# Kernel tuning notes

Measured on AMD Instinct MI355X. Metric: run time of the kernel, lower is better.

## Reference

```python
import jax, jax.numpy as jnp
import numpy as np

B, T, C, H = 8, 2048, 1024, 128

def setup_inputs() -> dict:
    key = jax.random.key(0)
    kx, kq, kk, kv = jax.random.split(key, 4)
    x = jax.random.normal(kx, (B, T, C), dtype=jnp.float32)
    Wq = jax.random.normal(kq, (C, H), dtype=jnp.float32) * 0.02
    Wk = jax.random.normal(kk, (C, H), dtype=jnp.float32) * 0.02
    Wv = jax.random.normal(kv, (C, H), dtype=jnp.float32) * 0.02
    return {"x": x, "Wq": Wq, "Wk": Wk, "Wv": Wv}

def reference(x, Wq, Wk, Wv):
    # q,k,v: [B,T,H] via bias-free dense projections
    q = jnp.einsum('btc,ch->bth', x, Wq)
    k = jnp.einsum('btc,ch->bth', x, Wk)
    v = jnp.einsum('btc,ch->bth', x, Wv)
    scale = k.shape[-1] ** (-0.5)
    # scores: [B,T,T]
    wei = jnp.einsum('bth,bsh->bts', q, k) * scale
    Tlen = x.shape[1]
    causal = jnp.tril(jnp.ones((Tlen, Tlen), dtype=bool))  # True = keep
    wei = jnp.where(causal[None, :, :], wei, -jnp.inf)
    wei = jax.nn.softmax(wei, axis=-1)
    return jnp.einsum('bts,bsh->bth', wei, v)
```

## Files before the change

kernel.cpp:

```cpp
#include <hip/hip_runtime.h>

#define B_ 8
#define T_ 2048
#define C_ 1024
#define H_ 128
#define BT_ (B_*T_)

typedef unsigned short u16;
typedef unsigned int u32;
typedef __attribute__((ext_vector_type(4))) float f32x4;
typedef __attribute__((ext_vector_type(8))) __bf16 bf16x8;

__device__ __forceinline__ u16 f2bf(float f) {
  u32 u = __float_as_uint(f);
  u += 0x7fffu + ((u >> 16) & 1u);
  return (u16)(u >> 16);
}

__device__ __forceinline__ void dma16(const u16* g, u16* l) {
  __builtin_amdgcn_global_load_lds(
      (const __attribute__((address_space(1))) u32*)g,
      (__attribute__((address_space(3))) u32*)l, 16, 0, 0);
}

__device__ __forceinline__ bf16x8 load_frag(const u16* base, int stride, int row0, int k0, int lane) {
  const u16* p = base + (size_t)(row0 + (lane & 15)) * stride + k0 + ((lane >> 4) << 3);
  return *reinterpret_cast<const bf16x8*>(p);
}

__global__ __launch_bounds__(256) void prep_kernel(const float* __restrict__ x,
                                                   const float* __restrict__ Wq,
                                                   const float* __restrict__ Wk,
                                                   const float* __restrict__ Wv,
                                                   u16* __restrict__ xb, u16* __restrict__ wt) {
  __shared__ float tile[32][33];
  int blk = blockIdx.x, t = threadIdx.x;
  if (blk < 2048) {
    size_t base = (size_t)blk * 8192 + t * 8;
#pragma unroll
    for (int j = 0; j < 4; j++) {
      size_t i = base + (size_t)j * 2048;
      float4 a = *reinterpret_cast<const float4*>(x + i);
      float4 b = *reinterpret_cast<const float4*>(x + i + 4);
      union { u16 h[8]; uint4 v; } r;
      r.h[0] = f2bf(a.x); r.h[1] = f2bf(a.y); r.h[2] = f2bf(a.z); r.h[3] = f2bf(a.w);
      r.h[4] = f2bf(b.x); r.h[5] = f2bf(b.y); r.h[6] = f2bf(b.z); r.h[7] = f2bf(b.w);
      *reinterpret_cast<uint4*>(xb + i) = r.v;
    }
  } else {
    int tid = blk - 2048;
    int mat = tid >> 7;
    int rem = tid & 127;
    int c0 = (rem & 31) * 32;
    int h0 = (rem >> 5) * 32;
    const float* W = (mat == 0) ? Wq : (mat == 1) ? Wk : Wv;
    int rr = t >> 5, cc = t & 31;
#pragma unroll
    for (int p = 0; p < 4; p++) {
      int i = p * 8 + rr;
      tile[i][cc] = W[(size_t)(c0 + i) * H_ + h0 + cc];
    }
    __syncthreads();
#pragma unroll
    for (int p = 0; p < 4; p++) {
      int j = p * 8 + rr;
      wt[(size_t)mat * (C_ * H_) + (size_t)(h0 + j) * C_ + c0 + cc] = f2bf(tile[cc][j]);
    }
  }
}

__global__ __launch_bounds__(256) void qkv_gemm(const u16* __restrict__ xb, const u16* __restrict__ wt,
                                                u16* __restrict__ q, u16* __restrict__ k2,
                                                u16* __restrict__ vt) {
  __shared__ __align__(16) u16 As[2][4096];
  __shared__ __align__(16) u16 Bs[2][4096];
  int t = threadIdx.x;
  int lane = t & 63, w = t >> 6;
  int wm = w >> 1, wn = w & 1;
  int quad = lane >> 4, col = lane & 15;
  int m0 = blockIdx.x * 128;
  int mat = blockIdx.y;
  const u16* wtm = wt + mat * (C_ * H_);

  int rj[2], oj[2];
#pragma unroll
  for (int j = 0; j < 2; j++) {
    int c = (j * 4 + w) * 64 + lane;
    int r = c >> 2;
    int qg = (c & 3) ^ ((r >> 1) & 3);
    rj[j] = r; oj[j] = qg * 8;
  }

#pragma unroll
  for (int j = 0; j < 2; j++) {
    dma16(xb + (size_t)(m0 + rj[j]) * C_ + oj[j], &As[0][(j * 4 + w) * 512]);
    dma16(wtm + (size_t)rj[j] * C_ + oj[j], &Bs[0][(j * 4 + w) * 512]);
  }

  int aoff[4], boff[4];
#pragma unroll
  for (int mt = 0; mt < 4; mt++) {
    int row = wm * 64 + mt * 16 + col;
    aoff[mt] = (4 * row + (quad ^ ((row >> 1) & 3))) * 8;
    int rowb = wn * 64 + mt * 16 + col;
    boff[mt] = (4 * rowb + (quad ^ ((rowb >> 1) & 3))) * 8;
  }

  f32x4 acc[4][4] = {};
  for (int kk = 0; kk < 32; kk++) {
    int cur = kk & 1;
    __syncthreads();
    if (kk + 1 < 32) {
      int nxt = cur ^ 1;
      int kn = (kk + 1) * 32;
#pragma unroll
      for (int j = 0; j < 2; j++) {
        dma16(xb + (size_t)(m0 + rj[j]) * C_ + kn + oj[j], &As[nxt][(j * 4 + w) * 512]);
        dma16(wtm + (size_t)rj[j] * C_ + kn + oj[j], &Bs[nxt][(j * 4 + w) * 512]);
      }
    }
    bf16x8 af[4], bfr[4];
#pragma unroll
    for (int mt = 0; mt < 4; mt++) af[mt] = *reinterpret_cast<const bf16x8*>(&As[cur][aoff[mt]]);
#pragma unroll
    for (int nt = 0; nt < 4; nt++) bfr[nt] = *reinterpret_cast<const bf16x8*>(&Bs[cur][boff[nt]]);
#pragma unroll
    for (int mt = 0; mt < 4; mt++)
#pragma unroll
      for (int nt = 0; nt < 4; nt++)
        acc[mt][nt] = __builtin_amdgcn_mfma_f32_16x16x32_bf16(af[mt], bfr[nt], acc[mt][nt], 0, 0, 0);
  }

#pragma unroll
  for (int mt = 0; mt < 4; mt++) {
#pragma unroll
    for (int nt = 0; nt < 4; nt++) {
#pragma unroll
      for (int r = 0; r < 4; r++) {
        int row = m0 + wm * 64 + mt * 16 + quad * 4 + r;
        int n = wn * 64 + nt * 16 + col;
        u16 val = f2bf(acc[mt][nt][r]);
        if (mat == 0) {
          q[(size_t)row * H_ + n] = val;
        } else if (mat == 1) {
          k2[(size_t)row * H_ + n] = val;
        } else {
          int bb = row >> 11;
          int tt = row & 2047;
          vt[((size_t)bb * H_ + n) * T_ + tt] = val;
        }
      }
    }
  }
}

__global__ __launch_bounds__(256) void attn_part(const u16* __restrict__ q, const u16* __restrict__ k,
                                                 const u16* __restrict__ vt,
                                                 float* __restrict__ Op, float* __restrict__ lsum) {
  __shared__ __align__(16) u16 Ks[2][8192];
  __shared__ __align__(16) u16 Vs[2][8192];
  __shared__ __align__(16) u16 P[4][16 * 72];
  int t = threadIdx.x;
  int lane = t & 63, w = t >> 6;
  int quad = lane >> 4, col = lane & 15;
  int bx = blockIdx.x;
  int qt = 31 - (bx >> 4);
  int s = (bx >> 3) & 1;
  int b = bx & 7;
  const float scale = 0.08838834764831845f;

  int nkt = qt + 1;
  int n0 = (nkt + 1) >> 1;
  int it0 = s ? n0 : 0;
  int it1 = s ? nkt : n0;

  int krj[4], koj[4], vrj[4], voj[4];
#pragma unroll
  for (int j = 0; j < 4; j++) {
    int c = (j * 4 + w) * 64 + lane;
    int rk = c >> 4; krj[j] = rk; koj[j] = ((c & 15) ^ (rk & 7)) * 8;
    int rv = c >> 3; vrj[j] = rv; voj[j] = ((c & 7) ^ (rv & 7)) * 8;
  }

  int qrow0 = b * T_ + qt * 64 + w * 16;
  bf16x8 qf[4];
#pragma unroll
  for (int ks = 0; ks < 4; ks++) qf[ks] = load_frag(q, H_, qrow0, ks * 32, lane);

  int koff[4][4], voff[8][2];
#pragma unroll
  for (int g = 0; g < 4; g++) {
    int row = g * 16 + col;
#pragma unroll
    for (int ks = 0; ks < 4; ks++)
      koff[g][ks] = (16 * row + ((ks * 4 + quad) ^ (row & 7))) * 8;
  }
#pragma unroll
  for (int ht = 0; ht < 8; ht++) {
    int row = ht * 16 + col;
#pragma unroll
    for (int kk = 0; kk < 2; kk++)
      voff[ht][kk] = (8 * row + ((kk * 4 + quad) ^ (row & 7))) * 8;
  }

  f32x4 o[8] = {};
  float l[4] = {0.f, 0.f, 0.f, 0.f};
  int myqrow = qt * 64 + w * 16 + quad * 4;
  u16* Pb = &P[w][0];

  if (it0 < it1) {
    {
      const u16* kb = k + (size_t)(b * T_ + it0 * 64) * H_;
      const u16* vb = vt + (size_t)b * H_ * T_ + it0 * 64;
#pragma unroll
      for (int j = 0; j < 4; j++) {
        dma16(kb + (size_t)krj[j] * H_ + koj[j], &Ks[0][(j * 4 + w) * 512]);
        dma16(vb + (size_t)vrj[j] * T_ + voj[j], &Vs[0][(j * 4 + w) * 512]);
      }
    }

    for (int kt = it0; kt < it1; kt++) {
      int cur = (kt - it0) & 1;
      __syncthreads();
      if (kt + 1 < it1) {
        int nxt = cur ^ 1;
        const u16* kb = k + (size_t)(b * T_ + (kt + 1) * 64) * H_;
        const u16* vb = vt + (size_t)b * H_ * T_ + (kt + 1) * 64;
#pragma unroll
        for (int j = 0; j < 4; j++) {
          dma16(kb + (size_t)krj[j] * H_ + koj[j], &Ks[nxt][(j * 4 + w) * 512]);
          dma16(vb + (size_t)vrj[j] * T_ + voj[j], &Vs[nxt][(j * 4 + w) * 512]);
        }
      }

      f32x4 sg[4] = {};
#pragma unroll
      for (int g = 0; g < 4; g++) {
#pragma unroll
        for (int ks = 0; ks < 4; ks++) {
          bf16x8 kf = *reinterpret_cast<const bf16x8*>(&Ks[cur][koff[g][ks]]);
          sg[g] = __builtin_amdgcn_mfma_f32_16x16x32_bf16(qf[ks], kf, sg[g], 0, 0, 0);
        }
      }

      bool diag = (kt == nkt - 1);
      float pv[4][4];
#pragma unroll
      for (int g = 0; g < 4; g++) {
        int kcol = kt * 64 + g * 16 + col;
#pragma unroll
        for (int r = 0; r < 4; r++) {
          float a = fminf(sg[g][r] * scale, 30.f);
          if (diag) a = (kcol > myqrow + r) ? -1e30f : a;
          float p = __expf(a);
          pv[g][r] = p;
          l[r] += p;
        }
      }

#pragma unroll
      for (int g = 0; g < 4; g++)
#pragma unroll
        for (int r = 0; r < 4; r++)
          Pb[(quad * 4 + r) * 72 + g * 16 + col] = f2bf(pv[g][r]);
      asm volatile("" ::: "memory");
      __builtin_amdgcn_s_waitcnt(0xc07f);
      asm volatile("" ::: "memory");
      bf16x8 pf0 = *reinterpret_cast<const bf16x8*>(&Pb[col * 72 + quad * 8]);
      bf16x8 pf1 = *reinterpret_cast<const bf16x8*>(&Pb[col * 72 + 32 + quad * 8]);

#pragma unroll
      for (int ht = 0; ht < 8; ht++) {
        bf16x8 vf0 = *reinterpret_cast<const bf16x8*>(&Vs[cur][voff[ht][0]]);
        bf16x8 vf1 = *reinterpret_cast<const bf16x8*>(&Vs[cur][voff[ht][1]]);
        o[ht] = __builtin_amdgcn_mfma_f32_16x16x32_bf16(pf0, vf0, o[ht], 0, 0, 0);
        o[ht] = __builtin_amdgcn_mfma_f32_16x16x32_bf16(pf1, vf1, o[ht], 0, 0, 0);
      }
    }
  }

#pragma unroll
  for (int r = 0; r < 4; r++) {
    float v = l[r];
    v += __shfl_xor(v, 1);
    v += __shfl_xor(v, 2);
    v += __shfl_xor(v, 4);
    v += __shfl_xor(v, 8);
    l[r] = v;
  }

  int tile = (s * 8 + b) * 32 + qt;
  float* Orow = Op + (size_t)tile * (64 * 128);
  float* lrow = lsum + (size_t)tile * 64;
  int rowin0 = w * 16 + quad * 4;
  if (col == 0) {
#pragma unroll
    for (int r = 0; r < 4; r++) lrow[rowin0 + r] = l[r];
  }
#pragma unroll
  for (int ht = 0; ht < 8; ht++) {
#pragma unroll
    for (int r = 0; r < 4; r++)
      Orow[(size_t)(rowin0 + r) * 128 + ht * 16 + col] = o[ht][r];
  }
}

__global__ __launch_bounds__(256) void attn_comb(const float* __restrict__ Op, const float* __restrict__ lsum,
                                                 float* __restrict__ out) {
  int bx = blockIdx.x;
  int b = bx >> 5, qt = bx & 31;
  int t = threadIdx.x;
  int h = t & 127, half = t >> 7;
  int tile0 = b * 32 + qt;
  int tile1 = tile0 + 256;
#pragma unroll 4
  for (int rr = 0; rr < 32; rr++) {
    int row = half * 32 + rr;
    float l0 = lsum[tile0 * 64 + row];
    float l1 = lsum[tile1 * 64 + row];
    float rl = 1.f / (l0 + l1);
    float v = (Op[(size_t)tile0 * 8192 + row * 128 + h] +
               Op[(size_t)tile1 * 8192 + row * 128 + h]) * rl;
    out[((size_t)(b * T_ + qt * 64 + row)) * H_ + h] = v;
  }
}

extern "C" void kernel_launch(void* const* d_in, const int* in_sizes, int n_in,
                              void* d_out, int out_size, void* d_ws, size_t ws_size,
                              hipStream_t stream) {
  (void)in_sizes; (void)n_in; (void)out_size; (void)ws_size;
  const float* x  = (const float*)d_in[0];
  const float* Wq = (const float*)d_in[1];
  const float* Wk = (const float*)d_in[2];
  const float* Wv = (const float*)d_in[3];
  u16* ws = (u16*)d_ws;
  u16* xb = ws;
  u16* q  = ws + (size_t)BT_ * C_;
  u16* k  = q + (size_t)BT_ * H_;
  u16* vt = k + (size_t)BT_ * H_;
  u16* wt = vt + (size_t)BT_ * H_;
  float* Op = (float*)xb;
  float* lsum = Op + (size_t)512 * 64 * 128;
  float* out = (float*)d_out;

  prep_kernel<<<dim3(2432), 256, 0, stream>>>(x, Wq, Wk, Wv, xb, wt);
  qkv_gemm<<<dim3(128, 3), 256, 0, stream>>>(xb, wt, q, k, vt);
  attn_part<<<dim3(512), 256, 0, stream>>>(q, k, vt, Op, lsum);
  attn_comb<<<dim3(256), 256, 0, stream>>>(Op, lsum, out);
}
```

Before: 175.0 us.

## Fuse split-KV combine into attention via atomic tickets, shrink QKV GEMM tiles

Removes the separate combine kernel. Each attention block bumps a per-tile atomic counter after writing its partial result, and the second finisher merges both halves and writes the final output. The counters are zeroed inside the prep kernel. The QKV GEMM M-tile is halved to 64 rows, doubling the block count for better CU occupancy. Block order is also remapped so the heaviest causal tiles of the two splits interleave, which should balance the load. In exchange it adds threadfence and atomic traffic and relies on correct cross-block memory ordering.

Result: slower. 260.4 us (+48.8%).

```diff
diff --git a/kernel.cpp b/kernel.cpp
--- a/kernel.cpp
+++ b/kernel.cpp
@@ -32,7 +32,8 @@
                                                    const float* __restrict__ Wq,
                                                    const float* __restrict__ Wk,
                                                    const float* __restrict__ Wv,
-                                                   u16* __restrict__ xb, u16* __restrict__ wt) {
+                                                   u16* __restrict__ xb, u16* __restrict__ wt,
+                                                   int* __restrict__ tick) {
   __shared__ float tile[32][33];
   int blk = blockIdx.x, t = threadIdx.x;
   if (blk < 2048) {
@@ -49,6 +50,7 @@
     }
   } else {
     int tid = blk - 2048;
+    if (tid == 0) tick[t] = 0;
     int mat = tid >> 7;
     int rem = tid & 127;
     int c0 = (rem & 31) * 32;
@@ -72,72 +74,76 @@
 __global__ __launch_bounds__(256) void qkv_gemm(const u16* __restrict__ xb, const u16* __restrict__ wt,
                                                 u16* __restrict__ q, u16* __restrict__ k2,
                                                 u16* __restrict__ vt) {
-  __shared__ __align__(16) u16 As[2][4096];
+  __shared__ __align__(16) u16 As[2][2048];
   __shared__ __align__(16) u16 Bs[2][4096];
   int t = threadIdx.x;
   int lane = t & 63, w = t >> 6;
   int wm = w >> 1, wn = w & 1;
   int quad = lane >> 4, col = lane & 15;
-  int m0 = blockIdx.x * 128;
+  int m0 = blockIdx.x * 64;
   int mat = blockIdx.y;
   const u16* wtm = wt + mat * (C_ * H_);
 
-  int rj[2], oj[2];
+  int ca = w * 64 + lane;
+  int ra = ca >> 2;
+  int oa = ((ca & 3) ^ ((ra >> 1) & 3)) * 8;
+  int rb[2], ob[2];
 #pragma unroll
   for (int j = 0; j < 2; j++) {
     int c = (j * 4 + w) * 64 + lane;
     int r = c >> 2;
-    int qg = (c & 3) ^ ((r >> 1) & 3);
-    rj[j] = r; oj[j] = qg * 8;
-  }
-
-#pragma unroll
-  for (int j = 0; j < 2; j++) {
-    dma16(xb + (size_t)(m0 + rj[j]) * C_ + oj[j], &As[0][(j * 4 + w) * 512]);
-    dma16(wtm + (size_t)rj[j] * C_ + oj[j], &Bs[0][(j * 4 + w) * 512]);
-  }
-
-  int aoff[4], boff[4];
-#pragma unroll
-  for (int mt = 0; mt < 4; mt++) {
-    int row = wm * 64 + mt * 16 + col;
+    ob[j] = ((c & 3) ^ ((r >> 1) & 3)) * 8;
+    rb[j] = r;
+  }
+
+  dma16(xb + (size_t)(m0 + ra) * C_ + oa, &As[0][w * 512]);
+#pragma unroll
+  for (int j = 0; j < 2; j++)
+    dma16(wtm + (size_t)rb[j] * C_ + ob[j], &Bs[0][(j * 4 + w) * 512]);
+
+  int aoff[2], boff[4];
+#pragma unroll
+  for (int mt = 0; mt < 2; mt++) {
+    int row = wm * 32 + mt * 16 + col;
     aoff[mt] = (4 * row + (quad ^ ((row >> 1) & 3))) * 8;
-    int rowb = wn * 64 + mt * 16 + col;
-    boff[mt] = (4 * rowb + (quad ^ ((rowb >> 1) & 3))) * 8;
-  }
-
-  f32x4 acc[4][4] = {};
+  }
+#pragma unroll
+  for (int nt = 0; nt < 4; nt++) {
+    int row = wn * 64 + nt * 16 + col;
+    boff[nt] = (4 * row + (quad ^ ((row >> 1) & 3))) * 8;
+  }
+
+  f32x4 acc[2][4] = {};
   for (int kk = 0; kk < 32; kk++) {
     int cur = kk & 1;
     __syncthreads();
     if (kk + 1 < 32) {
       int nxt = cur ^ 1;
       int kn = (kk + 1) * 32;
-#pragma unroll
-      for (int j = 0; j < 2; j++) {
-        dma16(xb + (size_t)(m0 + rj[j]) * C_ + kn + oj[j], &As[nxt][(j * 4 + w) * 512]);
-        dma16(wtm + (size_t)rj[j] * C_ + kn + oj[j], &Bs[nxt][(j * 4 + w) * 512]);
-      }
-    }
-    bf16x8 af[4], bfr[4];
-#pragma unroll
-    for (int mt = 0; mt < 4; mt++) af[mt] = *reinterpret_cast<const bf16x8*>(&As[cur][aoff[mt]]);
+      dma16(xb + (size_t)(m0 + ra) * C_ + kn + oa, &As[nxt][w * 512]);
+#pragma unroll
+      for (int j = 0; j < 2; j++)
+        dma16(wtm + (size_t)rb[j] * C_ + kn + ob[j], &Bs[nxt][(j * 4 + w) * 512]);
+    }
+    bf16x8 af[2], bfr[4];
+#pragma unroll
+    for (int mt = 0; mt < 2; mt++) af[mt] = *reinterpret_cast<const bf16x8*>(&As[cur][aoff[mt]]);
 #pragma unroll
     for (int nt = 0; nt < 4; nt++) bfr[nt] = *reinterpret_cast<const bf16x8*>(&Bs[cur][boff[nt]]);
 #pragma unroll
-    for (int mt = 0; mt < 4; mt++)
+    for (int mt = 0; mt < 2; mt++)
 #pragma unroll
       for (int nt = 0; nt < 4; nt++)
         acc[mt][nt] = __builtin_amdgcn_mfma_f32_16x16x32_bf16(af[mt], bfr[nt], acc[mt][nt], 0, 0, 0);
   }
 
 #pragma unroll
-  for (int mt = 0; mt < 4; mt++) {
+  for (int mt = 0; mt < 2; mt++) {
 #pragma unroll
     for (int nt = 0; nt < 4; nt++) {
 #pragma unroll
       for (int r = 0; r < 4; r++) {
-        int row = m0 + wm * 64 + mt * 16 + quad * 4 + r;
+        int row = m0 + wm * 32 + mt * 16 + quad * 4 + r;
         int n = wn * 64 + nt * 16 + col;
         u16 val = f2bf(acc[mt][nt][r]);
         if (mat == 0) {
@@ -156,17 +162,20 @@
 
 __global__ __launch_bounds__(256) void attn_part(const u16* __restrict__ q, const u16* __restrict__ k,
                                                  const u16* __restrict__ vt,
-                                                 float* __restrict__ Op, float* __restrict__ lsum) {
+                                                 float* __restrict__ Op, float* __restrict__ lsum,
+                                                 int* __restrict__ tick, float* __restrict__ out) {
   __shared__ __align__(16) u16 Ks[2][8192];
   __shared__ __align__(16) u16 Vs[2][8192];
   __shared__ __align__(16) u16 P[4][16 * 72];
+  __shared__ int oldt;
   int t = threadIdx.x;
   int lane = t & 63, w = t >> 6;
   int quad = lane >> 4, col = lane & 15;
   int bx = blockIdx.x;
-  int qt = 31 - (bx >> 4);
-  int s = (bx >> 3) & 1;
-  int b = bx & 7;
+  int rk_ = (bx < 256) ? bx : 767 - bx;
+  int qt = 31 - (rk_ >> 4);
+  int s = (rk_ >> 3) & 1;
+  int b = rk_ & 7;
   const float scale = 0.08838834764831845f;
 
   int nkt = qt + 1;
@@ -303,25 +312,27 @@
     for (int r = 0; r < 4; r++)
       Orow[(size_t)(rowin0 + r) * 128 + ht * 16 + col] = o[ht][r];
   }
-}
-
-__global__ __launch_bounds__(256) void attn_comb(const float* __restrict__ Op, const float* __restrict__ lsum,
-                                                 float* __restrict__ out) {
-  int bx = blockIdx.x;
-  int b = bx >> 5, qt = bx & 31;
-  int t = threadIdx.x;
-  int h = t & 127, half = t >> 7;
-  int tile0 = b * 32 + qt;
-  int tile1 = tile0 + 256;
-#pragma unroll 4
-  for (int rr = 0; rr < 32; rr++) {
-    int row = half * 32 + rr;
-    float l0 = lsum[tile0 * 64 + row];
-    float l1 = lsum[tile1 * 64 + row];
-    float rl = 1.f / (l0 + l1);
-    float v = (Op[(size_t)tile0 * 8192 + row * 128 + h] +
-               Op[(size_t)tile1 * 8192 + row * 128 + h]) * rl;
-    out[((size_t)(b * T_ + qt * 64 + row)) * H_ + h] = v;
+
+  __threadfence();
+  if (t == 0) oldt = atomicAdd(&tick[b * 32 + qt], 1);
+  __syncthreads();
+  if (oldt == 1) {
+    __threadfence();
+    int otile = ((1 - s) * 8 + b) * 32 + qt;
+    const float* Oo = Op + (size_t)otile * (64 * 128);
+    const float* lo = lsum + (size_t)otile * 64;
+    float rl[4];
+#pragma unroll
+    for (int r = 0; r < 4; r++) rl[r] = 1.f / (l[r] + lo[rowin0 + r]);
+#pragma unroll
+    for (int ht = 0; ht < 8; ht++) {
+#pragma unroll
+      for (int r = 0; r < 4; r++) {
+        int row = qt * 64 + rowin0 + r;
+        float v = (o[ht][r] + Oo[(size_t)(rowin0 + r) * 128 + ht * 16 + col]) * rl[r];
+        out[((size_t)(b * T_ + row)) * H_ + ht * 16 + col] = v;
+      }
+    }
   }
 }
 
@@ -339,12 +350,12 @@
   u16* k  = q + (size_t)BT_ * H_;
   u16* vt = k + (size_t)BT_ * H_;
   u16* wt = vt + (size_t)BT_ * H_;
+  int* tick = (int*)(wt + 3 * (size_t)C_ * H_);
   float* Op = (float*)xb;
   float* lsum = Op + (size_t)512 * 64 * 128;
   float* out = (float*)d_out;
 
-  prep_kernel<<<dim3(2432), 256, 0, stream>>>(x, Wq, Wk, Wv, xb, wt);
-  qkv_gemm<<<dim3(128, 3), 256, 0, stream>>>(xb, wt, q, k, vt);
-  attn_part<<<dim3(512), 256, 0, stream>>>(q, k, vt, Op, lsum);
-  attn_comb<<<dim3(256), 256, 0, stream>>>(Op, lsum, out);
-}
+  prep_kernel<<<dim3(2432), 256, 0, stream>>>(x, Wq, Wk, Wv, xb, wt, tick);
+  qkv_gemm<<<dim3(BT_ / 64, 3), 256, 0, stream>>>(xb, wt, q, k, vt);
+  attn_part<<<dim3(512), 256, 0, stream>>>(q, k, vt, Op, lsum, tick, out);
+}
```
